# Kernel optimization log

Hardware: AMD Instinct MI355X
Metric: run time of the kernel (lower is better)

## Reference

```python
import jax, jax.numpy as jnp
import numpy as np

SEQ, BATCH, IN_CH = 4096, 8, 256
HID = 256
LOOKBACK, LOOKAHEAD = 1, 0
K = LOOKBACK + 1 + LOOKAHEAD  # conv kernel size = 2


def setup_inputs() -> dict:
    key = jax.random.key(0)
    k1, k2, k3, k4, k5, k6 = jax.random.split(key, 6)
    X = jax.random.normal(k1, (SEQ, BATCH, IN_CH), dtype=jnp.float32)
    hidden = jax.random.normal(k2, (BATCH, HID), dtype=jnp.float32)
    scale = 1.0 / np.sqrt(IN_CH * K)
    Wz = jax.random.normal(k3, (HID, IN_CH, K), dtype=jnp.float32) * scale
    bz = jax.random.normal(k4, (HID,), dtype=jnp.float32) * scale
    Wf = jax.random.normal(k5, (HID, IN_CH, K), dtype=jnp.float32) * scale
    bf = jax.random.normal(k6, (HID,), dtype=jnp.float32) * scale
    return {"X": X, "hidden": hidden, "Wz": Wz, "bz": bz, "Wf": Wf, "bf": bf}


def _conv1d(Xp, W, b):
    # Xp: (B, C_in, S_pad); W: (C_out, C_in, K) -> (B, C_out, S)
    y = jax.lax.conv_general_dilated(
        Xp, W, window_strides=(1,), padding='VALID',
        dimension_numbers=('NCW', 'OIW', 'NCW'))
    return y + b[None, :, None]


def reference(X, hidden, Wz, bz, Wf, bf):
    # pad seq dim: lookback zeros in front, lookahead behind
    X_pad = jnp.pad(X, ((LOOKBACK, LOOKAHEAD), (0, 0), (0, 0)))
    Xp = jnp.transpose(X_pad, (1, 2, 0))  # (B, C_in, S_pad)

    Z = jnp.transpose(_conv1d(Xp, Wz, bz), (2, 0, 1))  # (S, B, H)
    F = jnp.transpose(_conv1d(Xp, Wf, bf), (2, 0, 1))  # (S, B, H)

    Z = Z * jax.nn.sigmoid(1.702 * Z)  # QuickGELU
    F = jax.nn.sigmoid(F)

    def step(h, fz):
        f, z = fz
        h = f * z + (1.0 - f) * h
        return h, h

    h_last, H = jax.lax.scan(step, hidden, (F, Z))
    return H, h_last[None]  # (S,B,H), (1,B,H)
```

## Files before the change

### kernel.cpp

```cpp
#include <hip/hip_runtime.h>


#define SEQn 4096
#define NCH 2048
#define CHUNK 32
#define NCHUNK 128

typedef __attribute__((ext_vector_type(8))) short bf16x8;
typedef __attribute__((ext_vector_type(4))) float floatx4;

__device__ __forceinline__ unsigned short f2bf(float x) {
  unsigned int u = __float_as_uint(x);
  u += 0x7fffu + ((u >> 16) & 1u);
  return (unsigned short)(u >> 16);
}
__device__ __forceinline__ float bf2f(ushort u) {
  return __uint_as_float((unsigned int)u << 16);
}
__device__ __forceinline__ float sigf(float x) {
  return __builtin_amdgcn_rcpf(1.0f + __expf(-x));
}
__device__ __forceinline__ float qgelu(float x) {
  return x * sigf(1.702f * x);
}

__global__ void pack_kernel(const float* __restrict__ X,
                            const float* __restrict__ Wz, const float* __restrict__ Wf,
                            ushort* __restrict__ Xbf, ushort* __restrict__ Bm) {
  if (blockIdx.x < 1024) {
    int idx = blockIdx.x * 256 + threadIdx.x;
    int n = idx >> 9, kin = idx & 511;
    const float* W = (n < 256) ? Wz : Wf;
    int h = n & 255, c = kin & 255, tap = kin >> 8;
    Bm[idx] = f2bf(W[h * 512 + c * 2 + tap]);
  } else {
    int idx = (blockIdx.x - 1024) * 256 + threadIdx.x;
    const int total4 = ((SEQn + 1) * NCH) / 4;
    if (idx >= total4) return;
    const int pad4 = NCH / 4;
    float4 v;
    if (idx < pad4) { v.x = 0.f; v.y = 0.f; v.z = 0.f; v.w = 0.f; }
    else v = ((const float4*)X)[idx - pad4];
    ushort4 o;
    o.x = f2bf(v.x); o.y = f2bf(v.y); o.z = f2bf(v.z); o.w = f2bf(v.w);
    ((ushort4*)Xbf)[idx] = o;
  }
}

__global__ __launch_bounds__(256) void gemm_kernel(
    const ushort* __restrict__ Xbf, const ushort* __restrict__ Bm,
    ushort* __restrict__ zout, ushort* __restrict__ fout) {
  __shared__ __align__(16) char smem_raw[32768];
  ushort* sA = (ushort*)smem_raw;
  ushort* sB = (ushort*)(smem_raw + 16384);
  ushort* sT = (ushort*)smem_raw;

  const int tid  = threadIdx.x;
  const int wave = tid >> 6;
  const int lane = tid & 63;
  const int quad = lane >> 4;
  const int lrow = lane & 15;
  const int wm = wave >> 1;
  const int wn = wave & 1;
  const int bm = blockIdx.x;
  const int bn = blockIdx.y;

  floatx4 acc[4][4];
#pragma unroll
  for (int i = 0; i < 4; ++i)
#pragma unroll
    for (int j = 0; j < 4; ++j)
      acc[i][j] = (floatx4){0.f, 0.f, 0.f, 0.f};

  int rowS[4], gko[4];
#pragma unroll
  for (int it = 0; it < 4; ++it) {
    int g = wave * 256 + it * 64 + lane;
    int row = g >> 3, ks8 = g & 7;
    rowS[it] = row;
    gko[it] = (ks8 ^ (row & 7)) * 8;
  }
  char* ldsA = (char*)sA + wave * 4096 + (lane << 4);
  char* ldsB = (char*)sB + wave * 4096 + (lane << 4);

  for (int k0 = 0; k0 < 512; k0 += 64) {
    __syncthreads();
#pragma unroll
    for (int it = 0; it < 4; ++it) {
      const int kk = k0 + gko[it];
      const int cA = (kk < 256) ? kk : kk + 1792;
      __builtin_amdgcn_global_load_lds(
          (const __attribute__((address_space(1))) void*)(Xbf + (size_t)(bm * 128 + rowS[it]) * 256 + cA),
          (__attribute__((address_space(3))) void*)(ldsA + it * 1024), 16, 0, 0);
      __builtin_amdgcn_global_load_lds(
          (const __attribute__((address_space(1))) void*)(Bm + (size_t)(bn * 128 + rowS[it]) * 512 + kk),
          (__attribute__((address_space(3))) void*)(ldsB + it * 1024), 16, 0, 0);
    }
    __syncthreads();

    bf16x8 af[4][2], bfr[4][2];
#pragma unroll
    for (int fi = 0; fi < 4; ++fi) {
      const int r = wm * 64 + fi * 16 + lrow;
#pragma unroll
      for (int ks = 0; ks < 2; ++ks) {
        const int s = (ks * 4 + quad) ^ (r & 7);
        af[fi][ks] = *(const bf16x8*)&sA[r * 64 + s * 8];
      }
    }
#pragma unroll
    for (int fj = 0; fj < 4; ++fj) {
      const int r = wn * 64 + fj * 16 + lrow;
#pragma unroll
      for (int ks = 0; ks < 2; ++ks) {
        const int s = (ks * 4 + quad) ^ (r & 7);
        bfr[fj][ks] = *(const bf16x8*)&sB[r * 64 + s * 8];
      }
    }
#pragma unroll
    for (int ks = 0; ks < 2; ++ks)
#pragma unroll
      for (int fi = 0; fi < 4; ++fi)
#pragma unroll
        for (int fj = 0; fj < 4; ++fj)
          acc[fi][fj] = __builtin_amdgcn_mfma_f32_16x16x32_bf16(af[fi][ks], bfr[fj][ks], acc[fi][fj], 0, 0, 0);
  }

  const bool isZ = (bn < 2);
  ushort* gout = isZ ? zout : fout;
  const int ncol0 = (bn & 1) * 128;

  for (int round = 0; round < 2; ++round) {
    __syncthreads();
    if (wm == round) {
#pragma unroll
      for (int fi = 0; fi < 4; ++fi)
#pragma unroll
        for (int fj = 0; fj < 4; ++fj)
#pragma unroll
          for (int r = 0; r < 4; ++r)
            sT[(fi * 16 + quad * 4 + r) * 136 + wn * 64 + fj * 16 + lrow] = f2bf(acc[fi][fj][r]);
    }
    __syncthreads();
#pragma unroll
    for (int it = 0; it < 4; ++it) {
      int e = tid + it * 256;
      int row = e >> 4, seg = e & 15;
      uint4 v = *(uint4*)&sT[row * 136 + seg * 8];
      *(uint4*)(gout + (size_t)(bm * 128 + round * 64 + row) * 256 + ncol0 + seg * 8) = v;
    }
  }
}

__global__ void scanA_kernel(const ushort* __restrict__ z, const ushort* __restrict__ f,
                             const float* __restrict__ bz, const float* __restrict__ bfb,
                             float* __restrict__ Ac, float* __restrict__ Cc) {
  int t = blockIdx.x * blockDim.x + threadIdx.x;
  int ch2 = t & 1023;
  int j = t >> 10;
  const int h0 = (2 * ch2) & 255, h1 = h0 + 1;
  const float zb0 = bz[h0], zb1 = bz[h1];
  const float fb0 = bfb[h0], fb1 = bfb[h1];
  const size_t base = (size_t)j * CHUNK * NCH + 2 * ch2;
  const ushort* zp = z + base;
  const ushort* fp = f + base;
  float A0 = 1.0f, C0 = 0.0f, A1 = 1.0f, C1 = 0.0f;
#pragma unroll
  for (int i = 0; i < CHUNK; ++i) {
    ushort2 fv = *(const ushort2*)(fp + (size_t)i * NCH);
    ushort2 zv = *(const ushort2*)(zp + (size_t)i * NCH);
    float f0 = sigf(bf2f(fv.x) + fb0), f1 = sigf(bf2f(fv.y) + fb1);
    float z0 = qgelu(bf2f(zv.x) + zb0), z1 = qgelu(bf2f(zv.y) + zb1);
    float a0 = 1.0f - f0, a1 = 1.0f - f1;
    C0 = fmaf(a0, C0, f0 * z0); A0 *= a0;
    C1 = fmaf(a1, C1, f1 * z1); A1 *= a1;
  }
  float2 Av = {A0, A1}, Cv = {C0, C1};
  *(float2*)(Ac + (size_t)j * NCH + 2 * ch2) = Av;
  *(float2*)(Cc + (size_t)j * NCH + 2 * ch2) = Cv;
}

__global__ void scanB_kernel(const float* __restrict__ hidden,
                             const float* __restrict__ Ac, const float* __restrict__ Cc,
                             float* __restrict__ Hs) {
  const int lane = threadIdx.x & 63;
  const int ch = blockIdx.x * 4 + (threadIdx.x >> 6);
  const int j0 = 2 * lane, j1 = 2 * lane + 1;
  float a0 = Ac[j0 * NCH + ch], c0 = Cc[j0 * NCH + ch];
  float a1 = Ac[j1 * NCH + ch], c1 = Cc[j1 * NCH + ch];
  float a = a0 * a1;
  float c = fmaf(a1, c0, c1);
#pragma unroll
  for (int d = 1; d < 64; d <<= 1) {
    float pa = __shfl_up(a, d, 64);
    float pc = __shfl_up(c, d, 64);
    if (lane >= d) { c = fmaf(a, pc, c); a *= pa; }
  }
  float xa = __shfl_up(a, 1, 64), xc = __shfl_up(c, 1, 64);
  if (lane == 0) { xa = 1.0f; xc = 0.0f; }
  float h0 = hidden[ch];
  float hs0 = fmaf(xa, h0, xc);
  Hs[j0 * NCH + ch] = hs0;
  Hs[j1 * NCH + ch] = fmaf(a0, hs0, c0);
}

__global__ void scanC_kernel(const ushort* __restrict__ z, const ushort* __restrict__ f,
                             const float* __restrict__ bz, const float* __restrict__ bfb,
                             const float* __restrict__ Hs, float* __restrict__ out) {
  int t = blockIdx.x * blockDim.x + threadIdx.x;
  int ch2 = t & 1023;
  int j = t >> 10;
  const int h0i = (2 * ch2) & 255, h1i = h0i + 1;
  const float zb0 = bz[h0i], zb1 = bz[h1i];
  const float fb0 = bfb[h0i], fb1 = bfb[h1i];
  float2 hv = *(const float2*)(Hs + (size_t)j * NCH + 2 * ch2);
  float h0 = hv.x, h1 = hv.y;
  const size_t base = (size_t)j * CHUNK * NCH + 2 * ch2;
  const ushort* zp = z + base;
  const ushort* fp = f + base;
  float* op = out + base;
#pragma unroll
  for (int i = 0; i < CHUNK; ++i) {
    ushort2 fv = *(const ushort2*)(fp + (size_t)i * NCH);
    ushort2 zv = *(const ushort2*)(zp + (size_t)i * NCH);
    float f0 = sigf(bf2f(fv.x) + fb0), f1 = sigf(bf2f(fv.y) + fb1);
    float z0 = qgelu(bf2f(zv.x) + zb0), z1 = qgelu(bf2f(zv.y) + zb1);
    h0 = fmaf(f0, z0 - h0, h0);
    h1 = fmaf(f1, z1 - h1, h1);
    float2 o = {h0, h1};
    *(float2*)(op + (size_t)i * NCH) = o;
  }
  if (j == NCHUNK - 1) {
    float2 o = {h0, h1};
    *(float2*)(out + (size_t)SEQn * NCH + 2 * ch2) = o;
  }
}

extern "C" void kernel_launch(void* const* d_in, const int* in_sizes, int n_in,
                              void* d_out, int out_size, void* d_ws, size_t ws_size,
                              hipStream_t stream) {
  const float* X      = (const float*)d_in[0];
  const float* hidden = (const float*)d_in[1];
  const float* Wz     = (const float*)d_in[2];
  const float* bz     = (const float*)d_in[3];
  const float* Wf     = (const float*)d_in[4];
  const float* bfb    = (const float*)d_in[5];
  float* out = (float*)d_out;

  char* ws = (char*)d_ws;
  ushort* zbf = (ushort*)ws;
  ushort* fbf = (ushort*)(ws + 16777216);
  ushort* Xbf = (ushort*)(ws + 33554432);
  ushort* Bm  = (ushort*)(ws + 50335744);
  float* Ac = (float*)(ws + 33554432);
  float* Cc = (float*)(ws + 34603008);
  float* Hs = (float*)(ws + 35651584);

  pack_kernel<<<9218, 256, 0, stream>>>(X, Wz, Wf, Xbf, Bm);
  dim3 ggrid(256, 4);
  gemm_kernel<<<ggrid, 256, 0, stream>>>(Xbf, Bm, zbf, fbf);
  scanA_kernel<<<512, 256, 0, stream>>>(zbf, fbf, bz, bfb, Ac, Cc);
  scanB_kernel<<<512, 256, 0, stream>>>(hidden, Ac, Cc, Hs);
  scanC_kernel<<<512, 256, 0, stream>>>(zbf, fbf, bz, bfb, Hs, out);
}
```

Measured before the change: 164.0 us.

## Load GEMM fragments directly from global into registers with double buffering

Removes the LDS staging of A and B tiles in the conv GEMM kernel. Each wave now loads its MFMA fragments straight from global memory into registers, with a two-deep register prefetch across 16 k-steps, and the per-iteration block barriers go away. The cost is redundant global/L2 traffic, since waves sharing rows or columns each load the same data, plus less coalesced 16-byte loads and more register pressure.

```diff
diff --git a/kernel.cpp b/kernel.cpp
--- a/kernel.cpp
+++ b/kernel.cpp
@@ -50,10 +50,7 @@
 __global__ __launch_bounds__(256) void gemm_kernel(
     const ushort* __restrict__ Xbf, const ushort* __restrict__ Bm,
     ushort* __restrict__ zout, ushort* __restrict__ fout) {
-  __shared__ __align__(16) char smem_raw[32768];
-  ushort* sA = (ushort*)smem_raw;
-  ushort* sB = (ushort*)(smem_raw + 16384);
-  ushort* sT = (ushort*)smem_raw;
+  __shared__ __align__(16) ushort sT[64 * 136];
 
   const int tid  = threadIdx.x;
   const int wave = tid >> 6;
@@ -65,6 +62,9 @@
   const int bm = blockIdx.x;
   const int bn = blockIdx.y;
 
+  const ushort* Abase = Xbf + (size_t)(bm * 128 + wm * 64 + lrow) * 256;
+  const ushort* Bbase = Bm  + (size_t)(bn * 128 + wn * 64 + lrow) * 512;
+
   floatx4 acc[4][4];
 #pragma unroll
   for (int i = 0; i < 4; ++i)
@@ -72,58 +72,35 @@
     for (int j = 0; j < 4; ++j)
       acc[i][j] = (floatx4){0.f, 0.f, 0.f, 0.f};
 
-  int rowS[4], gko[4];
-#pragma unroll
-  for (int it = 0; it < 4; ++it) {
-    int g = wave * 256 + it * 64 + lane;
-    int row = g >> 3, ks8 = g & 7;
-    rowS[it] = row;
-    gko[it] = (ks8 ^ (row & 7)) * 8;
-  }
-  char* ldsA = (char*)sA + wave * 4096 + (lane << 4);
-  char* ldsB = (char*)sB + wave * 4096 + (lane << 4);
-
-  for (int k0 = 0; k0 < 512; k0 += 64) {
-    __syncthreads();
-#pragma unroll
-    for (int it = 0; it < 4; ++it) {
-      const int kk = k0 + gko[it];
+  bf16x8 a[2][4], b[2][4];
+  {
+    const int kk = quad * 8;
+#pragma unroll
+    for (int fi = 0; fi < 4; ++fi)
+      a[0][fi] = *(const bf16x8*)(Abase + fi * 4096 + kk);
+#pragma unroll
+    for (int fj = 0; fj < 4; ++fj)
+      b[0][fj] = *(const bf16x8*)(Bbase + fj * 8192 + kk);
+  }
+
+#pragma unroll
+  for (int k = 0; k < 16; ++k) {
+    const int cur = k & 1, nxt = cur ^ 1;
+    if (k < 15) {
+      const int kk = (k + 1) * 32 + quad * 8;
       const int cA = (kk < 256) ? kk : kk + 1792;
-      __builtin_amdgcn_global_load_lds(
-          (const __attribute__((address_space(1))) void*)(Xbf + (size_t)(bm * 128 + rowS[it]) * 256 + cA),
-          (__attribute__((address_space(3))) void*)(ldsA + it * 1024), 16, 0, 0);
-      __builtin_amdgcn_global_load_lds(
-          (const __attribute__((address_space(1))) void*)(Bm + (size_t)(bn * 128 + rowS[it]) * 512 + kk),
-          (__attribute__((address_space(3))) void*)(ldsB + it * 1024), 16, 0, 0);
+#pragma unroll
+      for (int fi = 0; fi < 4; ++fi)
+        a[nxt][fi] = *(const bf16x8*)(Abase + fi * 4096 + cA);
+#pragma unroll
+      for (int fj = 0; fj < 4; ++fj)
+        b[nxt][fj] = *(const bf16x8*)(Bbase + fj * 8192 + kk);
     }
-    __syncthreads();
-
-    bf16x8 af[4][2], bfr[4][2];
-#pragma unroll
-    for (int fi = 0; fi < 4; ++fi) {
-      const int r = wm * 64 + fi * 16 + lrow;
-#pragma unroll
-      for (int ks = 0; ks < 2; ++ks) {
-        const int s = (ks * 4 + quad) ^ (r & 7);
-        af[fi][ks] = *(const bf16x8*)&sA[r * 64 + s * 8];
-      }
-    }
-#pragma unroll
-    for (int fj = 0; fj < 4; ++fj) {
-      const int r = wn * 64 + fj * 16 + lrow;
-#pragma unroll
-      for (int ks = 0; ks < 2; ++ks) {
-        const int s = (ks * 4 + quad) ^ (r & 7);
-        bfr[fj][ks] = *(const bf16x8*)&sB[r * 64 + s * 8];
-      }
-    }
-#pragma unroll
-    for (int ks = 0; ks < 2; ++ks)
-#pragma unroll
-      for (int fi = 0; fi < 4; ++fi)
-#pragma unroll
-        for (int fj = 0; fj < 4; ++fj)
-          acc[fi][fj] = __builtin_amdgcn_mfma_f32_16x16x32_bf16(af[fi][ks], bfr[fj][ks], acc[fi][fj], 0, 0, 0);
+#pragma unroll
+    for (int fi = 0; fi < 4; ++fi)
+#pragma unroll
+      for (int fj = 0; fj < 4; ++fj)
+        acc[fi][fj] = __builtin_amdgcn_mfma_f32_16x16x32_bf16(a[cur][fi], b[cur][fj], acc[fi][fj], 0, 0, 0);
   }
 
   const bool isZ = (bn < 2);
```

After: 186.5 us. 1.14x slower.
